# Kernel tuning notes

Measured on AMD Instinct MI355X. Metric: run time of the kernel, lower is better.

Reference implementation:

```python
import jax, jax.numpy as jnp
import numpy as np

# scipy.interpolate.splrep(x, y, s=0, k=3) on a uniform grid returns the
# interpolating cubic spline with not-a-knot boundary conditions (FITPACK
# places interior knots at x[2:-2]).  We therefore fit the not-a-knot cubic
# spline per row via a batched constant-coefficient Thomas solve and evaluate
# it at linspace(0, w-1, w*upsample_rate), matching splev(..., der=0).


def _notaknot_second_derivs(y):
    """Second derivatives M[b, i] of the not-a-knot cubic spline, uniform h=1.

    Interior eqs (i=1..w-2): M[i-1] + 4 M[i] + M[i+1] = 6*(y[i+1]-2y[i]+y[i-1])
    Not-a-knot: M[0]-2M[1]+M[2]=0 and M[w-3]-2M[w-2]+M[w-1]=0, which for a
    uniform grid decouples to M[1]=d[1]/6, M[w-2]=d[w-2]/6, leaving a plain
    [1,4,1] tridiagonal system for M[2..w-3].
    """
    B, w = y.shape
    d = 6.0 * (y[:, 2:] - 2.0 * y[:, 1:-1] + y[:, :-2])  # [B, w-2], i = 1..w-2
    M1 = d[:, 0] / 6.0    # M at index 1
    Mn2 = d[:, -1] / 6.0  # M at index w-2
    rhs = d[:, 1:-1]      # equations at i = 2..w-3, shape [B, m], m = w-4
    rhs = rhs.at[:, 0].add(-M1).at[:, -1].add(-Mn2)

    def fwd(carry, b):  # Thomas forward elimination, diag=4, off=1
        cp, dp = carry
        den = 4.0 - cp
        cp2 = 1.0 / den
        dp2 = (b - dp) / den
        return (cp2, dp2), (cp2, dp2)

    init = (jnp.zeros((), y.dtype), jnp.zeros((B,), y.dtype))
    _, (cps, dps) = jax.lax.scan(fwd, init, rhs.T)  # scan over length m

    def bwd(x_next, cd):  # back substitution
        cp, dp = cd
        x = dp - cp * x_next
        return x, x

    _, xs = jax.lax.scan(bwd, jnp.zeros((B,), y.dtype), (cps, dps), reverse=True)
    Mi = xs.T  # [B, m], M at indices 2..w-3

    # Extrapolate boundary second derivatives from the not-a-knot conditions.
    M0 = 2.0 * M1 - Mi[:, 0]
    Mw1 = 2.0 * Mn2 - Mi[:, -1]
    return jnp.concatenate(
        [M0[:, None], M1[:, None], Mi, Mn2[:, None], Mw1[:, None]], axis=1
    )  # [B, w]


def _spline_eval(y, M, upsample_rate):
    B, w = y.shape
    xq = jnp.linspace(0.0, w - 1.0, w * upsample_rate, dtype=y.dtype)  # [wq]
    i = jnp.clip(jnp.floor(xq).astype(jnp.int32), 0, w - 2)
    t = xq - i.astype(y.dtype)  # local coordinate in [0, 1]
    y0 = y[:, i]
    y1 = y[:, i + 1]
    M0 = M[:, i]
    M1 = M[:, i + 1]
    # f(t) = y0 + b t + M0/2 t^2 + (M1-M0)/6 t^3, with h=1
    b = (y1 - y0) - (2.0 * M0 + M1) / 6.0
    return y0 + t * (b + t * (0.5 * M0 + t * (M1 - M0) / 6.0))


def setup_inputs() -> dict:
    key = jax.random.key(0)
    x = jax.random.normal(key, (512, 8192), dtype=jnp.float32)
    return {"x": x, "upsample_rate": 4}


def reference(x, upsample_rate):
    M = _notaknot_second_derivs(x)
    return _spline_eval(x, M, upsample_rate)  # [B, w * upsample_rate]
```

## Files before the change

kernel.cpp:

```cpp
#include <hip/hip_runtime.h>


typedef float  f32x4 __attribute__((ext_vector_type(4)));
typedef float  f32x2 __attribute__((ext_vector_type(2)));

constexpr int W    = 8192;
constexpr int WU   = 32768;
constexpr int TILE = 512;
constexpr int HL   = 16;
constexpr int YSN  = 544;
constexpr int MSN  = 516;
constexpr int KB   = 10;
constexpr int BTN  = 538;

__global__ __launch_bounds__(256)
void spline_kernel(const float* __restrict__ x, float* __restrict__ out)
{
    const int row = blockIdx.y;
    const int s0  = blockIdx.x * TILE;
    const int tid = threadIdx.x;
    const int n   = W - 4;

    __shared__ __align__(16) float ys[YSN];
    __shared__ __align__(16) f32x2 ym[MSN];
    __shared__ float bt[BTN];

    const float* __restrict__ xr = x + (size_t)row * (size_t)W;
    const int YS0 = s0 - HL;

    if (tid < 128) {
        f32x4 v = *(const f32x4*)(xr + s0 + 4 * tid);
        *(f32x4*)&ys[HL + 4 * tid] = v;
    } else if (tid < 128 + 16) {
        int idx = tid - 128;
        int g = YS0 + idx; if (g < 0) g = 0;
        ys[idx] = xr[g];
    } else if (tid < 128 + 32) {
        int idx = tid - (128 + 16);
        int g = s0 + TILE + idx; if (g > W - 1) g = W - 1;
        ys[HL + TILE + idx] = xr[g];
    }
    __syncthreads();

    const bool boundary = (blockIdx.x == 0) || (blockIdx.x == gridDim.x - 1);

    if (!boundary) {
        if (tid < 129) {
            const f32x4* ys4 = (const f32x4*)ys;
            float w[32];
            #pragma unroll
            for (int k = 0; k < 8; ++k) {
                f32x4 v = ys4[tid + k];
                w[4*k+0] = v.x; w[4*k+1] = v.y; w[4*k+2] = v.z; w[4*k+3] = v.w;
            }
            float acc[4];
            #pragma unroll
            for (int c = 0; c < 4; ++c)
                acc[c] = -4.39230484541326386f * w[15 + c];
            float wd = 2.78460969082652752f;
            #pragma unroll
            for (int d = 1; d <= 12; ++d) {
                #pragma unroll
                for (int c = 0; c < 4; ++c)
                    acc[c] += wd * (w[15 + c - d] + w[15 + c + d]);
                wd *= -0.26794919243112270647f;
            }
            f32x4 o0 = {w[15], acc[0], w[16], acc[1]};
            f32x4 o1 = {w[17], acc[2], w[18], acc[3]};
            *(f32x4*)&ym[4 * tid]     = o0;
            *(f32x4*)&ym[4 * tid + 2] = o1;
        }
    } else {
        auto Dp = [&](int p) -> float {
            int a = p - YS0;
            return 6.0f * (ys[a + 1] - 2.0f * ys[a] + ys[a - 1]);
        };
        auto M1v = [&]() -> float {
            int a = -YS0; return ys[a] - 2.0f * ys[a + 1] + ys[a + 2];
        };
        auto Mn2v = [&]() -> float {
            int a = (W - 1) - YS0; return ys[a] - 2.0f * ys[a - 1] + ys[a - 2];
        };
        auto bval = [&](int m) -> float {
            if (m == -1 || m == n) return 0.0f;
            float sgn = 1.0f;
            if (m < -1)     { m = -2 - m;   sgn = -1.0f; }
            else if (m > n) { m = 2 * n - m; sgn = -1.0f; }
            float v = Dp(m + 2);
            if (m == 0)     v -= M1v();
            if (m == n - 1) v -= Mn2v();
            return sgn * v;
        };
        const int BT0 = s0 - 3 - KB;
        for (int idx = tid; idx < BTN; idx += 256)
            bt[idx] = bval(BT0 + idx);
        __syncthreads();
        auto convb = [&](int j) -> float {
            int base = j - 2 - BT0;
            float acc = 0.288675134594812882f * bt[base];
            float wr  = 0.288675134594812882f;
            #pragma unroll
            for (int d = 1; d <= KB; ++d) {
                wr  *= -0.26794919243112270647f;
                acc += wr * (bt[base - d] + bt[base + d]);
            }
            return acc;
        };
        for (int idx = tid; idx < MSN; idx += 256) {
            int j = s0 - 1 + idx;
            j = j < 0 ? 0 : (j > W - 1 ? W - 1 : j);
            float m;
            if (j == 0)          m = 2.0f * M1v() - convb(2);
            else if (j == 1)     m = M1v();
            else if (j == W - 2) m = Mn2v();
            else if (j == W - 1) m = 2.0f * Mn2v() - convb(W - 3);
            else                 m = convb(j);
            ym[idx] = (f32x2){ys[idx + 15], m};
        }
    }
    __syncthreads();

    float* __restrict__ orow = out + (size_t)row * (size_t)WU;
    const int qbase = s0 * (WU / W);
    #pragma unroll
    for (int it = 0; it < 2; ++it) {
        int q0  = qbase + (tid + it * 256) * 4;
        int num = q0 * (W - 1);
        int i0  = num / (WU - 1);
        int rr  = num - i0 * (WU - 1);
        int kM  = i0 - s0 + 1;
        f32x2 p0 = ym[kM], p1 = ym[kM + 1], p2 = ym[kM + 2];
        float res[4];
        int di = 0;
        #pragma unroll
        for (int u = 0; u < 4; ++u) {
            float t  = (float)rr * (1.0f / (float)(WU - 1));
            float y0 = di ? p1.x : p0.x;
            float y1 = di ? p2.x : p1.x;
            float m0 = di ? p1.y : p0.y;
            float m1 = di ? p2.y : p1.y;
            float bb = (y1 - y0) - (2.0f * m0 + m1) * (1.0f / 6.0f);
            res[u] = y0 + t * (bb + t * (0.5f * m0 + t * (m1 - m0) * (1.0f / 6.0f)));
            rr += (W - 1);
            if (rr >= WU - 1) { rr -= (WU - 1); di = 1; }
        }
        f32x4 o = (f32x4){res[0], res[1], res[2], res[3]};
        *(f32x4*)(orow + q0) = o;
    }
}

extern "C" void kernel_launch(void* const* d_in, const int* in_sizes, int n_in,
                              void* d_out, int out_size, void* d_ws, size_t ws_size,
                              hipStream_t stream) {
    const float* x = (const float*)d_in[0];
    float* out = (float*)d_out;
    const int B = in_sizes[0] / W;
    dim3 grid(W / TILE, B), block(256);
    hipLaunchKernelGGL(spline_kernel, grid, block, 0, stream, x, out);
}
```

Measured before the change: 27.27 us.

## Make blocks persistent per row, looping over tiles with register-prefetched halos

The grid now has one block per row instead of one per tile, and each block walks all tiles of its row. The next two tiles' inputs, halos included, are prefetched into registers while the current tile is computed, and a double-buffered shared array holds the input window. This is meant to hide global load latency and cut block launch overhead. The cost is a much smaller grid, 512 blocks of 256 threads, which may leave the memory system under-occupied on a large GPU.

```diff
diff --git a/kernel.cpp b/kernel.cpp
--- a/kernel.cpp
+++ b/kernel.cpp
@@ -1,12 +1,13 @@
 #include <hip/hip_runtime.h>
 
 
-typedef float  f32x4 __attribute__((ext_vector_type(4)));
-typedef float  f32x2 __attribute__((ext_vector_type(2)));
+typedef float f32x4 __attribute__((ext_vector_type(4)));
+typedef float f32x2 __attribute__((ext_vector_type(2)));
 
 constexpr int W    = 8192;
 constexpr int WU   = 32768;
 constexpr int TILE = 512;
+constexpr int NT   = W / TILE;
 constexpr int HL   = 16;
 constexpr int YSN  = 544;
 constexpr int MSN  = 516;
@@ -16,136 +17,159 @@
 __global__ __launch_bounds__(256)
 void spline_kernel(const float* __restrict__ x, float* __restrict__ out)
 {
-    const int row = blockIdx.y;
-    const int s0  = blockIdx.x * TILE;
+    const int row = blockIdx.x;
     const int tid = threadIdx.x;
     const int n   = W - 4;
+    const float* __restrict__ xr   = x   + (size_t)row * W;
+    float*       __restrict__ orow = out + (size_t)row * WU;
 
-    __shared__ __align__(16) float ys[YSN];
+    __shared__ __align__(16) float ys[2][YSN];
     __shared__ __align__(16) f32x2 ym[MSN];
     __shared__ float bt[BTN];
 
-    const float* __restrict__ xr = x + (size_t)row * (size_t)W;
-    const int YS0 = s0 - HL;
+    auto LOAD = [&](int tile) -> f32x4 {
+        f32x4 v = {0.f, 0.f, 0.f, 0.f};
+        if (tid < 136) {
+            int base = tile * TILE - HL + 4 * tid;
+            if (tile == 0 || tile == NT - 1) {
+                #pragma unroll
+                for (int e = 0; e < 4; ++e) {
+                    int g = base + e;
+                    g = g < 0 ? 0 : (g > W - 1 ? W - 1 : g);
+                    v[e] = xr[g];
+                }
+            } else {
+                v = *(const f32x4*)(xr + base);
+            }
+        }
+        return v;
+    };
 
-    if (tid < 128) {
-        f32x4 v = *(const f32x4*)(xr + s0 + 4 * tid);
-        *(f32x4*)&ys[HL + 4 * tid] = v;
-    } else if (tid < 128 + 16) {
-        int idx = tid - 128;
-        int g = YS0 + idx; if (g < 0) g = 0;
-        ys[idx] = xr[g];
-    } else if (tid < 128 + 32) {
-        int idx = tid - (128 + 16);
-        int g = s0 + TILE + idx; if (g > W - 1) g = W - 1;
-        ys[HL + TILE + idx] = xr[g];
-    }
+    f32x4 regA = LOAD(0);
+    if (tid < 136) *(f32x4*)&ys[0][4 * tid] = regA;
     __syncthreads();
+    regA = LOAD(1);
+    int cur = 0;
 
-    const bool boundary = (blockIdx.x == 0) || (blockIdx.x == gridDim.x - 1);
+    for (int k = 0; k < NT; ++k) {
+        f32x4 regB = {0.f, 0.f, 0.f, 0.f};
+        if (k + 2 < NT) regB = LOAD(k + 2);
 
-    if (!boundary) {
-        if (tid < 129) {
-            const f32x4* ys4 = (const f32x4*)ys;
-            float w[32];
-            #pragma unroll
-            for (int k = 0; k < 8; ++k) {
-                f32x4 v = ys4[tid + k];
-                w[4*k+0] = v.x; w[4*k+1] = v.y; w[4*k+2] = v.z; w[4*k+3] = v.w;
-            }
-            float acc[4];
-            #pragma unroll
-            for (int c = 0; c < 4; ++c)
-                acc[c] = -4.39230484541326386f * w[15 + c];
-            float wd = 2.78460969082652752f;
-            #pragma unroll
-            for (int d = 1; d <= 12; ++d) {
+        const int s0  = k * TILE;
+        const int YS0 = s0 - HL;
+        float* ysc = ys[cur];
+        const bool boundary = (k == 0) || (k == NT - 1);
+
+        if (!boundary) {
+            if (tid < 129) {
+                const f32x4* ys4 = (const f32x4*)ysc;
+                float w[32];
+                #pragma unroll
+                for (int kk = 0; kk < 8; ++kk) {
+                    f32x4 v = ys4[tid + kk];
+                    w[4*kk+0]=v.x; w[4*kk+1]=v.y; w[4*kk+2]=v.z; w[4*kk+3]=v.w;
+                }
+                float acc[4];
                 #pragma unroll
                 for (int c = 0; c < 4; ++c)
-                    acc[c] += wd * (w[15 + c - d] + w[15 + c + d]);
-                wd *= -0.26794919243112270647f;
+                    acc[c] = -4.39230484541326386f * w[15 + c];
+                float wd = 2.78460969082652752f;
+                #pragma unroll
+                for (int d = 1; d <= 12; ++d) {
+                    #pragma unroll
+                    for (int c = 0; c < 4; ++c)
+                        acc[c] += wd * (w[15 + c - d] + w[15 + c + d]);
+                    wd *= -0.26794919243112270647f;
+                }
+                f32x4 o0 = {w[15], acc[0], w[16], acc[1]};
+                f32x4 o1 = {w[17], acc[2], w[18], acc[3]};
+                *(f32x4*)&ym[4 * tid]     = o0;
+                *(f32x4*)&ym[4 * tid + 2] = o1;
             }
-            f32x4 o0 = {w[15], acc[0], w[16], acc[1]};
-            f32x4 o1 = {w[17], acc[2], w[18], acc[3]};
-            *(f32x4*)&ym[4 * tid]     = o0;
-            *(f32x4*)&ym[4 * tid + 2] = o1;
+        } else {
+            auto Dp = [&](int p) -> float {
+                int a = p - YS0;
+                return 6.0f * (ysc[a + 1] - 2.0f * ysc[a] + ysc[a - 1]);
+            };
+            auto M1v = [&]() -> float {
+                int a = -YS0; return ysc[a] - 2.0f * ysc[a + 1] + ysc[a + 2];
+            };
+            auto Mn2v = [&]() -> float {
+                int a = (W - 1) - YS0;
+                return ysc[a] - 2.0f * ysc[a - 1] + ysc[a - 2];
+            };
+            auto bval = [&](int m) -> float {
+                if (m == -1 || m == n) return 0.f;
+                float sgn = 1.f;
+                if (m < -1)     { m = -2 - m;    sgn = -1.f; }
+                else if (m > n) { m = 2 * n - m; sgn = -1.f; }
+                float v = Dp(m + 2);
+                if (m == 0)     v -= M1v();
+                if (m == n - 1) v -= Mn2v();
+                return sgn * v;
+            };
+            const int BT0 = s0 - 3 - KB;
+            for (int idx = tid; idx < BTN; idx += 256)
+                bt[idx] = bval(BT0 + idx);
+            __syncthreads();
+            auto convb = [&](int j) -> float {
+                int base = j - 2 - BT0;
+                float acc = 0.288675134594812882f * bt[base];
+                float wr  = 0.288675134594812882f;
+                #pragma unroll
+                for (int d = 1; d <= KB; ++d) {
+                    wr  *= -0.26794919243112270647f;
+                    acc += wr * (bt[base - d] + bt[base + d]);
+                }
+                return acc;
+            };
+            for (int idx = tid; idx < MSN; idx += 256) {
+                int j = s0 - 1 + idx;
+                j = j < 0 ? 0 : (j > W - 1 ? W - 1 : j);
+                float m;
+                if (j == 0)          m = 2.f*M1v()  - convb(2);
+                else if (j == 1)     m = M1v();
+                else if (j == W - 2) m = Mn2v();
+                else if (j == W - 1) m = 2.f*Mn2v() - convb(W - 3);
+                else                 m = convb(j);
+                ym[idx] = (f32x2){ysc[idx + 15], m};
+            }
         }
-    } else {
-        auto Dp = [&](int p) -> float {
-            int a = p - YS0;
-            return 6.0f * (ys[a + 1] - 2.0f * ys[a] + ys[a - 1]);
-        };
-        auto M1v = [&]() -> float {
-            int a = -YS0; return ys[a] - 2.0f * ys[a + 1] + ys[a + 2];
-        };
-        auto Mn2v = [&]() -> float {
-            int a = (W - 1) - YS0; return ys[a] - 2.0f * ys[a - 1] + ys[a - 2];
-        };
-        auto bval = [&](int m) -> float {
-            if (m == -1 || m == n) return 0.0f;
-            float sgn = 1.0f;
-            if (m < -1)     { m = -2 - m;   sgn = -1.0f; }
-            else if (m > n) { m = 2 * n - m; sgn = -1.0f; }
-            float v = Dp(m + 2);
-            if (m == 0)     v -= M1v();
-            if (m == n - 1) v -= Mn2v();
-            return sgn * v;
-        };
-        const int BT0 = s0 - 3 - KB;
-        for (int idx = tid; idx < BTN; idx += 256)
-            bt[idx] = bval(BT0 + idx);
         __syncthreads();
-        auto convb = [&](int j) -> float {
-            int base = j - 2 - BT0;
-            float acc = 0.288675134594812882f * bt[base];
-            float wr  = 0.288675134594812882f;
+
+        const int qbase = s0 * (WU / W);
+        #pragma unroll
+        for (int it = 0; it < 2; ++it) {
+            int q0  = qbase + (tid + it * 256) * 4;
+            int num = q0 * (W - 1);
+            int i0  = num / (WU - 1);
+            int rr  = num - i0 * (WU - 1);
+            int kM  = i0 - s0 + 1;
+            f32x2 p0 = ym[kM], p1 = ym[kM + 1], p2 = ym[kM + 2];
+            float res[4];
+            int di = 0;
             #pragma unroll
-            for (int d = 1; d <= KB; ++d) {
-                wr  *= -0.26794919243112270647f;
-                acc += wr * (bt[base - d] + bt[base + d]);
+            for (int u = 0; u < 4; ++u) {
+                float t  = (float)rr * (1.0f / (float)(WU - 1));
+                float y0 = di ? p1.x : p0.x;
+                float y1 = di ? p2.x : p1.x;
+                float m0 = di ? p1.y : p0.y;
+                float m1 = di ? p2.y : p1.y;
+                float bb = (y1 - y0) - (2.f*m0 + m1) * (1.f/6.f);
+                res[u] = y0 + t * (bb + t * (0.5f*m0 + t * (m1 - m0) * (1.f/6.f)));
+                rr += (W - 1);
+                if (rr >= WU - 1) { rr -= (WU - 1); di = 1; }
             }
-            return acc;
-        };
-        for (int idx = tid; idx < MSN; idx += 256) {
-            int j = s0 - 1 + idx;
-            j = j < 0 ? 0 : (j > W - 1 ? W - 1 : j);
-            float m;
-            if (j == 0)          m = 2.0f * M1v() - convb(2);
-            else if (j == 1)     m = M1v();
-            else if (j == W - 2) m = Mn2v();
-            else if (j == W - 1) m = 2.0f * Mn2v() - convb(W - 3);
-            else                 m = convb(j);
-            ym[idx] = (f32x2){ys[idx + 15], m};
+            f32x4 o = {res[0], res[1], res[2], res[3]};
+            *(f32x4*)(orow + q0) = o;
         }
-    }
-    __syncthreads();
 
-    float* __restrict__ orow = out + (size_t)row * (size_t)WU;
-    const int qbase = s0 * (WU / W);
-    #pragma unroll
-    for (int it = 0; it < 2; ++it) {
-        int q0  = qbase + (tid + it * 256) * 4;
-        int num = q0 * (W - 1);
-        int i0  = num / (WU - 1);
-        int rr  = num - i0 * (WU - 1);
-        int kM  = i0 - s0 + 1;
-        f32x2 p0 = ym[kM], p1 = ym[kM + 1], p2 = ym[kM + 2];
-        float res[4];
-        int di = 0;
-        #pragma unroll
-        for (int u = 0; u < 4; ++u) {
-            float t  = (float)rr * (1.0f / (float)(WU - 1));
-            float y0 = di ? p1.x : p0.x;
-            float y1 = di ? p2.x : p1.x;
-            float m0 = di ? p1.y : p0.y;
-            float m1 = di ? p2.y : p1.y;
-            float bb = (y1 - y0) - (2.0f * m0 + m1) * (1.0f / 6.0f);
-            res[u] = y0 + t * (bb + t * (0.5f * m0 + t * (m1 - m0) * (1.0f / 6.0f)));
-            rr += (W - 1);
-            if (rr >= WU - 1) { rr -= (WU - 1); di = 1; }
+        if (k + 1 < NT) {
+            if (tid < 136) *(f32x4*)&ys[cur ^ 1][4 * tid] = regA;
         }
-        f32x4 o = (f32x4){res[0], res[1], res[2], res[3]};
-        *(f32x4*)(orow + q0) = o;
+        __syncthreads();
+        regA = regB;
+        cur ^= 1;
     }
 }
 
@@ -155,6 +179,6 @@
     const float* x = (const float*)d_in[0];
     float* out = (float*)d_out;
     const int B = in_sizes[0] / W;
-    dim3 grid(W / TILE, B), block(256);
+    dim3 grid(B), block(256);
     hipLaunchKernelGGL(spline_kernel, grid, block, 0, stream, x, out);
 }
```

New measurement: 32.02 us. +17.4%, slower.
